# Kernel optimization log

Hardware: AMD Instinct MI355X
Metric: run time of the kernel (lower is better)

The kernel has to match this reference:

```python
import jax, jax.numpy as jnp
import numpy as np

B, S, D = 4, 2048, 1024  # batch, seq_len, isize; FFN hidden = isize, gate dim = 2*isize


def setup_inputs() -> dict:
    key = jax.random.key(0)
    ks = jax.random.split(key, 6)
    sc = lambda n: 1.0 / np.sqrt(n)
    return {
        "iQ": jax.random.normal(ks[0], (B, S, D), jnp.float32),
        "iV": jax.random.normal(ks[1], (B, S, D), jnp.float32),
        "W1": jax.random.normal(ks[2], (D, D), jnp.float32) * sc(D),
        "b1": jnp.zeros((D,), jnp.float32),
        "W2": jax.random.normal(ks[3], (D, D), jnp.float32) * sc(D),
        "b2": jnp.zeros((D,), jnp.float32),
        "Wg": jax.random.normal(ks[4], (2 * D, 2 * D), jnp.float32) * sc(2 * D),
        "bg": jnp.zeros((2 * D,), jnp.float32),
    }


def reference(iQ, iV, W1, b1, W2, b2, Wg, bg):
    seql = iV.shape[1]
    # AAN cumulative-average matrix: row i has 1/(i+1) in cols 0..i (lower triangular)
    inv = 1.0 / jnp.arange(1, seql + 1, dtype=iV.dtype)  # [S]
    attn = jnp.tril(jnp.broadcast_to(inv[:, None], (seql, seql)))  # [S, S]
    avg = jnp.einsum('st,btd->bsd', attn, iV)  # [B, S, D]
    # PositionwiseFF with norm_input=False, dropout=0: Linear -> ReLU -> Linear
    h = jax.nn.relu(avg @ W1 + b1)
    ffn = h @ W2 + b2  # [B, S, D]
    # sigmoid gate over concat(iQ, ffn)
    g = jax.nn.sigmoid(jnp.concatenate([iQ, ffn], axis=-1) @ Wg + bg)  # [B, S, 2D]
    d = ffn.shape[-1]
    igate = g[..., :d]
    fgate = g[..., d:]
    return igate * iQ + fgate * ffn
```

## Files before the change

kernel.cpp:

```cpp
#include <hip/hip_runtime.h>
#include <hip/hip_bf16.h>
#include <cstdint>

typedef unsigned short u16;
typedef unsigned int   u32;

typedef __attribute__((ext_vector_type(8))) short short8;
typedef __attribute__((ext_vector_type(4))) float f32x4;

__device__ __forceinline__ float b2f(u16 v) { return __uint_as_float(((u32)v) << 16); }
__device__ __forceinline__ u16 f2b(float f) {
    u32 u = __float_as_uint(f);
    u += 0x7FFFu + ((u >> 16) & 1u);
    return (u16)(u >> 16);
}

#define G2L16(gp, lp) __builtin_amdgcn_global_load_lds(                       \
    (const __attribute__((address_space(1))) void*)(gp),                      \
    (__attribute__((address_space(3))) void*)(lp), 16, 0, 0)

__device__ __forceinline__ void transpose_body(const float* __restrict__ in,
                                               u16* __restrict__ out,
                                               int R, int C, int lb, int tilesX,
                                               float (*tile)[33]) {
    const int bx = (lb % tilesX) * 32;
    const int by = (lb / tilesX) * 32;
    const int tx = threadIdx.x & 31, ty = threadIdx.x >> 5;
    #pragma unroll
    for (int i = 0; i < 32; i += 8)
        tile[ty + i][tx] = in[(size_t)(by + ty + i) * C + (bx + tx)];
    __syncthreads();
    #pragma unroll
    for (int i = 0; i < 32; i += 8)
        out[(size_t)(bx + ty + i) * R + (by + tx)] = f2b(tile[tx][ty + i]);
}

__global__ void prologue_kernel(const float* __restrict__ W1, u16* __restrict__ W1t,
                                const float* __restrict__ W2, u16* __restrict__ W2t,
                                const float* __restrict__ Wg, u16* __restrict__ Wgt,
                                const float* __restrict__ iQ, u16* __restrict__ iQb,
                                const float* __restrict__ iV, float* __restrict__ csum) {
    __shared__ float tile[32][33];
    const int bid = blockIdx.x;
    const int tid = threadIdx.x;
    if (bid < 1024) {
        transpose_body(W1, W1t, 1024, 1024, bid, 32, tile);
    } else if (bid < 2048) {
        transpose_body(W2, W2t, 1024, 1024, bid - 1024, 32, tile);
    } else if (bid < 6144) {
        transpose_body(Wg, Wgt, 2048, 2048, bid - 2048, 64, tile);
    } else if (bid < 14336) {
        const size_t i = ((size_t)(bid - 6144) * 256 + tid) * 4;
        const float4 v = *(const float4*)(iQ + i);
        ushort4 o;
        o.x = f2b(v.x); o.y = f2b(v.y); o.z = f2b(v.z); o.w = f2b(v.w);
        *(ushort4*)(iQb + i) = o;
    } else {
        const int idx = bid - 14336;
        const int b = idx >> 6, c = idx & 63;
        const int d = tid * 4;
        const float* src = iV + ((size_t)(b * 2048 + c * 32)) * 1024 + d;
        float4 s = {0.f, 0.f, 0.f, 0.f};
        #pragma unroll 8
        for (int i = 0; i < 32; ++i) {
            const float4 v = *(const float4*)(src + (size_t)i * 1024);
            s.x += v.x; s.y += v.y; s.z += v.z; s.w += v.w;
        }
        *(float4*)(csum + ((size_t)(b * 64 + c)) * 1024 + d) = s;
    }
}

__global__ void scan_kernel(const float* __restrict__ iV, const float* __restrict__ csum,
                            u16* __restrict__ avg) {
    const int c = blockIdx.x & 63, b = blockIdx.x >> 6;
    const int d = threadIdx.x * 4;
    float4 acc = {0.f, 0.f, 0.f, 0.f};
    const float* cs = csum + (size_t)b * 64 * 1024 + d;
    for (int cc = 0; cc < c; ++cc) {
        const float4 v = *(const float4*)(cs + (size_t)cc * 1024);
        acc.x += v.x; acc.y += v.y; acc.z += v.z; acc.w += v.w;
    }
    const size_t off = ((size_t)(b * 2048 + c * 32)) * 1024 + d;
    const float* src = iV + off;
    u16*         dst = avg + off;
    const int s0 = c * 32;
    #pragma unroll 4
    for (int i = 0; i < 32; ++i) {
        const float4 v = *(const float4*)(src + (size_t)i * 1024);
        acc.x += v.x; acc.y += v.y; acc.z += v.z; acc.w += v.w;
        const float inv = 1.0f / (float)(s0 + i + 1);
        ushort4 o;
        o.x = f2b(acc.x * inv); o.y = f2b(acc.y * inv);
        o.z = f2b(acc.z * inv); o.w = f2b(acc.w * inv);
        *(ushort4*)(dst + (size_t)i * 1024) = o;
    }
}

template <int EPI>
__global__ __launch_bounds__(256, 2)
void gemm_kernel(const u16* __restrict__ A, const u16* __restrict__ Bt,
                 const float* __restrict__ bias, u16* __restrict__ C,
                 int M, int N, int K) {
    __shared__ u16 As[128 * 32];
    __shared__ u16 Bs[128 * 32];

    const int tid  = threadIdx.x;
    const int m0   = blockIdx.x * 128;
    const int n0   = blockIdx.y * 128;
    const int wave = tid >> 6, lane = tid & 63;
    const int wm   = (wave & 1) << 6;
    const int wn   = (wave >> 1) << 6;
    const int quad = lane >> 4, l16 = lane & 15;

    f32x4 acc[4][4];
    #pragma unroll
    for (int i = 0; i < 4; ++i)
        #pragma unroll
        for (int j = 0; j < 4; ++j) acc[i][j] = (f32x4){0.f, 0.f, 0.f, 0.f};

    const int o1 = tid * 16, o2 = o1 + 4096;
    const int r1 = o1 >> 6, c1 = o1 & 63;
    const int r2 = o2 >> 6, c2 = o2 & 63;

    const int ktiles = K >> 5;
    for (int kt = 0; kt < ktiles; ++kt) {
        const int kb = kt << 5;
        const char* Ab = (const char*)(A + kb);
        const char* Bb = (const char*)(Bt + kb);
        G2L16(Ab + (size_t)(m0 + r1) * K * 2 + c1, (char*)As + o1);
        G2L16(Ab + (size_t)(m0 + r2) * K * 2 + c2, (char*)As + o2);
        G2L16(Bb + (size_t)(n0 + r1) * K * 2 + c1, (char*)Bs + o1);
        G2L16(Bb + (size_t)(n0 + r2) * K * 2 + c2, (char*)Bs + o2);
        __syncthreads();

        short8 af[4], bf[4];
        #pragma unroll
        for (int mi = 0; mi < 4; ++mi)
            af[mi] = *(const short8*)(As + (wm + mi * 16 + l16) * 32 + quad * 8);
        #pragma unroll
        for (int ni = 0; ni < 4; ++ni)
            bf[ni] = *(const short8*)(Bs + (wn + ni * 16 + l16) * 32 + quad * 8);
        #pragma unroll
        for (int mi = 0; mi < 4; ++mi)
            #pragma unroll
            for (int ni = 0; ni < 4; ++ni)
                acc[mi][ni] = __builtin_amdgcn_mfma_f32_16x16x32_bf16(
                    af[mi], bf[ni], acc[mi][ni], 0, 0, 0);
        __syncthreads();
    }

    #pragma unroll
    for (int ni = 0; ni < 4; ++ni) {
        const int col = n0 + wn + ni * 16 + l16;
        const float bv = bias[col];
        #pragma unroll
        for (int mi = 0; mi < 4; ++mi) {
            const int row0 = m0 + wm + mi * 16 + quad * 4;
            #pragma unroll
            for (int r = 0; r < 4; ++r) {
                float v = acc[mi][ni][r] + bv;
                if (EPI == 0) v = fmaxf(v, 0.f);
                C[(size_t)(row0 + r) * N + col] = f2b(v);
            }
        }
    }
}

__global__ __launch_bounds__(256, 2)
void gemm_gate_kernel(const u16* __restrict__ iQb, const u16* __restrict__ ffn,
                      const u16* __restrict__ Wgt, const float* __restrict__ bg,
                      const float* __restrict__ iQ, float* __restrict__ out,
                      int M, int D2 ) {
    __shared__ u16 As [128 * 32];
    __shared__ u16 Bs0[128 * 32];
    __shared__ u16 Bs1[128 * 32];

    const int tid  = threadIdx.x;
    const int m0   = blockIdx.x * 128;
    const int n0   = blockIdx.y * 128;
    const int wave = tid >> 6, lane = tid & 63;
    const int wm   = (wave & 1) << 6;
    const int wn   = (wave >> 1) << 6;
    const int quad = lane >> 4, l16 = lane & 15;
    const int D = D2 >> 1;

    f32x4 acc[2][4][4];
    #pragma unroll
    for (int p = 0; p < 2; ++p)
        #pragma unroll
        for (int i = 0; i < 4; ++i)
            #pragma unroll
            for (int j = 0; j < 4; ++j) acc[p][i][j] = (f32x4){0.f, 0.f, 0.f, 0.f};

    const int o1 = tid * 16, o2 = o1 + 4096;
    const int r1 = o1 >> 6, c1 = o1 & 63;
    const int r2 = o2 >> 6, c2 = o2 & 63;

    const int ktiles = D2 >> 5;
    for (int kt = 0; kt < ktiles; ++kt) {
        const int kb = kt << 5;
        const char* Ab = (const char*)((kb < D) ? (iQb + kb) : (ffn + (kb - D)));
        const char* B0 = (const char*)(Wgt + (size_t)n0 * D2 + kb);
        const char* B1 = (const char*)(Wgt + (size_t)(n0 + D) * D2 + kb);
        G2L16(Ab + (size_t)(m0 + r1) * D * 2 + c1, (char*)As + o1);
        G2L16(Ab + (size_t)(m0 + r2) * D * 2 + c2, (char*)As + o2);
        G2L16(B0 + (size_t)r1 * D2 * 2 + c1, (char*)Bs0 + o1);
        G2L16(B0 + (size_t)r2 * D2 * 2 + c2, (char*)Bs0 + o2);
        G2L16(B1 + (size_t)r1 * D2 * 2 + c1, (char*)Bs1 + o1);
        G2L16(B1 + (size_t)r2 * D2 * 2 + c2, (char*)Bs1 + o2);
        __syncthreads();

        short8 af[4], bf0[4], bf1[4];
        #pragma unroll
        for (int mi = 0; mi < 4; ++mi)
            af[mi] = *(const short8*)(As + (wm + mi * 16 + l16) * 32 + quad * 8);
        #pragma unroll
        for (int ni = 0; ni < 4; ++ni) {
            bf0[ni] = *(const short8*)(Bs0 + (wn + ni * 16 + l16) * 32 + quad * 8);
            bf1[ni] = *(const short8*)(Bs1 + (wn + ni * 16 + l16) * 32 + quad * 8);
        }
        #pragma unroll
        for (int mi = 0; mi < 4; ++mi)
            #pragma unroll
            for (int ni = 0; ni < 4; ++ni) {
                acc[0][mi][ni] = __builtin_amdgcn_mfma_f32_16x16x32_bf16(
                    af[mi], bf0[ni], acc[0][mi][ni], 0, 0, 0);
                acc[1][mi][ni] = __builtin_amdgcn_mfma_f32_16x16x32_bf16(
                    af[mi], bf1[ni], acc[1][mi][ni], 0, 0, 0);
            }
        __syncthreads();
    }

    #pragma unroll
    for (int ni = 0; ni < 4; ++ni) {
        const int col = n0 + wn + ni * 16 + l16;
        const float bgi = bg[col];
        const float bgf = bg[col + D];
        #pragma unroll
        for (int mi = 0; mi < 4; ++mi) {
            const int row0 = m0 + wm + mi * 16 + quad * 4;
            #pragma unroll
            for (int r = 0; r < 4; ++r) {
                const size_t idx = (size_t)(row0 + r) * D + col;
                const float gi = 1.0f / (1.0f + __expf(-(acc[0][mi][ni][r] + bgi)));
                const float gf = 1.0f / (1.0f + __expf(-(acc[1][mi][ni][r] + bgf)));
                out[idx] = gi * iQ[idx] + gf * b2f(ffn[idx]);
            }
        }
    }
}

extern "C" void kernel_launch(void* const* d_in, const int* in_sizes, int n_in,
                              void* d_out, int out_size, void* d_ws, size_t ws_size,
                              hipStream_t stream) {
    const int B = 4, S = 2048, D = 1024, D2 = 2048;
    const int M = B * S;

    const float* iQ = (const float*)d_in[0];
    const float* iV = (const float*)d_in[1];
    const float* W1 = (const float*)d_in[2];
    const float* b1 = (const float*)d_in[3];
    const float* W2 = (const float*)d_in[4];
    const float* b2 = (const float*)d_in[5];
    const float* Wg = (const float*)d_in[6];
    const float* bg = (const float*)d_in[7];
    float* out = (float*)d_out;

    u16*   regA = (u16*)d_ws;
    u16*   regB = regA + (size_t)M * D;
    u16*   iQb  = regB + (size_t)M * D;
    u16*   W1t  = iQb  + (size_t)M * D;
    u16*   W2t  = W1t  + (size_t)D * D;
    u16*   Wgt  = W2t  + (size_t)D * D;
    float* csum = (float*)(Wgt + (size_t)D2 * D2);

    u16* avg = regA;
    u16* ffn = regA;
    u16* h   = regB;

    prologue_kernel<<<14592, 256, 0, stream>>>(W1, W1t, W2, W2t, Wg, Wgt,
                                               iQ, iQb, iV, csum);
    scan_kernel<<<B * 64, 256, 0, stream>>>(iV, csum, avg);
    gemm_kernel<0><<<dim3(M / 128, D / 128), 256, 0, stream>>>(avg, W1t, b1, h, M, D, D);
    gemm_kernel<1><<<dim3(M / 128, D / 128), 256, 0, stream>>>(h, W2t, b2, ffn, M, D, D);
    gemm_gate_kernel<<<dim3(M / 128, D / 128), 256, 0, stream>>>(
        iQb, ffn, Wgt, bg, iQ, out, M, D2);
}
```

Before: 304.3 us.

## Double GEMM K-tile to 64 with XOR-swizzled LDS layout; unroll scan prefix

Both GEMM kernels now stage 64-wide K tiles instead of 32, which halves the number of barrier pairs per K loop. The shared-memory layout uses an XOR swizzle on 16-byte chunks so that MFMA fragment reads avoid bank conflicts. The scan kernel's chunk-prefix loop gets four independent accumulators to expose more memory-level parallelism. In exchange, LDS use doubles, reaching 48KB for the gate kernel, which may limit the two-blocks-per-CU occupancy.

```diff
diff --git a/kernel.cpp b/kernel.cpp
--- a/kernel.cpp
+++ b/kernel.cpp
@@ -74,12 +74,29 @@
                             u16* __restrict__ avg) {
     const int c = blockIdx.x & 63, b = blockIdx.x >> 6;
     const int d = threadIdx.x * 4;
-    float4 acc = {0.f, 0.f, 0.f, 0.f};
     const float* cs = csum + (size_t)b * 64 * 1024 + d;
-    for (int cc = 0; cc < c; ++cc) {
+    float4 a0 = {0,0,0,0}, a1 = {0,0,0,0}, a2 = {0,0,0,0}, a3 = {0,0,0,0};
+    int cc = 0;
+    for (; cc + 4 <= c; cc += 4) {
+        const float4 v0 = *(const float4*)(cs + (size_t)(cc + 0) * 1024);
+        const float4 v1 = *(const float4*)(cs + (size_t)(cc + 1) * 1024);
+        const float4 v2 = *(const float4*)(cs + (size_t)(cc + 2) * 1024);
+        const float4 v3 = *(const float4*)(cs + (size_t)(cc + 3) * 1024);
+        a0.x += v0.x; a0.y += v0.y; a0.z += v0.z; a0.w += v0.w;
+        a1.x += v1.x; a1.y += v1.y; a1.z += v1.z; a1.w += v1.w;
+        a2.x += v2.x; a2.y += v2.y; a2.z += v2.z; a2.w += v2.w;
+        a3.x += v3.x; a3.y += v3.y; a3.z += v3.z; a3.w += v3.w;
+    }
+    for (; cc < c; ++cc) {
         const float4 v = *(const float4*)(cs + (size_t)cc * 1024);
-        acc.x += v.x; acc.y += v.y; acc.z += v.z; acc.w += v.w;
-    }
+        a0.x += v.x; a0.y += v.y; a0.z += v.z; a0.w += v.w;
+    }
+    float4 acc;
+    acc.x = (a0.x + a1.x) + (a2.x + a3.x);
+    acc.y = (a0.y + a1.y) + (a2.y + a3.y);
+    acc.z = (a0.z + a1.z) + (a2.z + a3.z);
+    acc.w = (a0.w + a1.w) + (a2.w + a3.w);
+
     const size_t off = ((size_t)(b * 2048 + c * 32)) * 1024 + d;
     const float* src = iV + off;
     u16*         dst = avg + off;
@@ -101,8 +118,8 @@
 void gemm_kernel(const u16* __restrict__ A, const u16* __restrict__ Bt,
                  const float* __restrict__ bias, u16* __restrict__ C,
                  int M, int N, int K) {
-    __shared__ u16 As[128 * 32];
-    __shared__ u16 Bs[128 * 32];
+    __shared__ u16 As[128 * 64];
+    __shared__ u16 Bs[128 * 64];
 
     const int tid  = threadIdx.x;
     const int m0   = blockIdx.x * 128;
@@ -118,34 +135,46 @@
         #pragma unroll
         for (int j = 0; j < 4; ++j) acc[i][j] = (f32x4){0.f, 0.f, 0.f, 0.f};
 
-    const int o1 = tid * 16, o2 = o1 + 4096;
-    const int r1 = o1 >> 6, c1 = o1 & 63;
-    const int r2 = o2 >> 6, c2 = o2 & 63;
-
-    const int ktiles = K >> 5;
+    int oo[4], rr[4], qq[4];
+    #pragma unroll
+    for (int j = 0; j < 4; ++j) {
+        oo[j] = tid * 16 + j * 4096;
+        rr[j] = oo[j] >> 7;
+        qq[j] = ((oo[j] >> 4) & 7) ^ (rr[j] & 7);
+    }
+
+    const int ktiles = K >> 6;
     for (int kt = 0; kt < ktiles; ++kt) {
-        const int kb = kt << 5;
-        const char* Ab = (const char*)(A + kb);
-        const char* Bb = (const char*)(Bt + kb);
-        G2L16(Ab + (size_t)(m0 + r1) * K * 2 + c1, (char*)As + o1);
-        G2L16(Ab + (size_t)(m0 + r2) * K * 2 + c2, (char*)As + o2);
-        G2L16(Bb + (size_t)(n0 + r1) * K * 2 + c1, (char*)Bs + o1);
-        G2L16(Bb + (size_t)(n0 + r2) * K * 2 + c2, (char*)Bs + o2);
+        const int kb = kt << 6;
+        #pragma unroll
+        for (int j = 0; j < 4; ++j) {
+            G2L16((const char*)A  + ((size_t)(m0 + rr[j]) * K + kb) * 2 + qq[j] * 16,
+                  (char*)As + oo[j]);
+            G2L16((const char*)Bt + ((size_t)(n0 + rr[j]) * K + kb) * 2 + qq[j] * 16,
+                  (char*)Bs + oo[j]);
+        }
         __syncthreads();
 
-        short8 af[4], bf[4];
-        #pragma unroll
-        for (int mi = 0; mi < 4; ++mi)
-            af[mi] = *(const short8*)(As + (wm + mi * 16 + l16) * 32 + quad * 8);
-        #pragma unroll
-        for (int ni = 0; ni < 4; ++ni)
-            bf[ni] = *(const short8*)(Bs + (wn + ni * 16 + l16) * 32 + quad * 8);
-        #pragma unroll
-        for (int mi = 0; mi < 4; ++mi)
-            #pragma unroll
-            for (int ni = 0; ni < 4; ++ni)
-                acc[mi][ni] = __builtin_amdgcn_mfma_f32_16x16x32_bf16(
-                    af[mi], bf[ni], acc[mi][ni], 0, 0, 0);
+        #pragma unroll
+        for (int h = 0; h < 2; ++h) {
+            short8 af[4], bf[4];
+            #pragma unroll
+            for (int mi = 0; mi < 4; ++mi) {
+                const int R = wm + mi * 16 + l16;
+                af[mi] = *(const short8*)(As + R * 64 + ((((h << 2) | quad) ^ (R & 7)) << 3));
+            }
+            #pragma unroll
+            for (int ni = 0; ni < 4; ++ni) {
+                const int R = wn + ni * 16 + l16;
+                bf[ni] = *(const short8*)(Bs + R * 64 + ((((h << 2) | quad) ^ (R & 7)) << 3));
+            }
+            #pragma unroll
+            for (int mi = 0; mi < 4; ++mi)
+                #pragma unroll
+                for (int ni = 0; ni < 4; ++ni)
+                    acc[mi][ni] = __builtin_amdgcn_mfma_f32_16x16x32_bf16(
+                        af[mi], bf[ni], acc[mi][ni], 0, 0, 0);
+        }
         __syncthreads();
     }
 
@@ -171,9 +200,9 @@
                       const u16* __restrict__ Wgt, const float* __restrict__ bg,
                       const float* __restrict__ iQ, float* __restrict__ out,
                       int M, int D2 ) {
-    __shared__ u16 As [128 * 32];
-    __shared__ u16 Bs0[128 * 32];
-    __shared__ u16 Bs1[128 * 32];
+    __shared__ u16 As [128 * 64];
+    __shared__ u16 Bs0[128 * 64];
+    __shared__ u16 Bs1[128 * 64];
 
     const int tid  = threadIdx.x;
     const int m0   = blockIdx.x * 128;
@@ -192,42 +221,53 @@
             #pragma unroll
             for (int j = 0; j < 4; ++j) acc[p][i][j] = (f32x4){0.f, 0.f, 0.f, 0.f};
 
-    const int o1 = tid * 16, o2 = o1 + 4096;
-    const int r1 = o1 >> 6, c1 = o1 & 63;
-    const int r2 = o2 >> 6, c2 = o2 & 63;
-
-    const int ktiles = D2 >> 5;
+    int oo[4], rr[4], qq[4];
+    #pragma unroll
+    for (int j = 0; j < 4; ++j) {
+        oo[j] = tid * 16 + j * 4096;
+        rr[j] = oo[j] >> 7;
+        qq[j] = ((oo[j] >> 4) & 7) ^ (rr[j] & 7);
+    }
+
+    const int ktiles = D2 >> 6;
     for (int kt = 0; kt < ktiles; ++kt) {
-        const int kb = kt << 5;
+        const int kb = kt << 6;
         const char* Ab = (const char*)((kb < D) ? (iQb + kb) : (ffn + (kb - D)));
         const char* B0 = (const char*)(Wgt + (size_t)n0 * D2 + kb);
         const char* B1 = (const char*)(Wgt + (size_t)(n0 + D) * D2 + kb);
-        G2L16(Ab + (size_t)(m0 + r1) * D * 2 + c1, (char*)As + o1);
-        G2L16(Ab + (size_t)(m0 + r2) * D * 2 + c2, (char*)As + o2);
-        G2L16(B0 + (size_t)r1 * D2 * 2 + c1, (char*)Bs0 + o1);
-        G2L16(B0 + (size_t)r2 * D2 * 2 + c2, (char*)Bs0 + o2);
-        G2L16(B1 + (size_t)r1 * D2 * 2 + c1, (char*)Bs1 + o1);
-        G2L16(B1 + (size_t)r2 * D2 * 2 + c2, (char*)Bs1 + o2);
+        #pragma unroll
+        for (int j = 0; j < 4; ++j) {
+            G2L16(Ab + (size_t)(m0 + rr[j]) * D * 2 + qq[j] * 16, (char*)As  + oo[j]);
+            G2L16(B0 + (size_t)rr[j] * D2 * 2 + qq[j] * 16,       (char*)Bs0 + oo[j]);
+            G2L16(B1 + (size_t)rr[j] * D2 * 2 + qq[j] * 16,       (char*)Bs1 + oo[j]);
+        }
         __syncthreads();
 
-        short8 af[4], bf0[4], bf1[4];
-        #pragma unroll
-        for (int mi = 0; mi < 4; ++mi)
-            af[mi] = *(const short8*)(As + (wm + mi * 16 + l16) * 32 + quad * 8);
-        #pragma unroll
-        for (int ni = 0; ni < 4; ++ni) {
-            bf0[ni] = *(const short8*)(Bs0 + (wn + ni * 16 + l16) * 32 + quad * 8);
-            bf1[ni] = *(const short8*)(Bs1 + (wn + ni * 16 + l16) * 32 + quad * 8);
-        }
-        #pragma unroll
-        for (int mi = 0; mi < 4; ++mi)
+        #pragma unroll
+        for (int h = 0; h < 2; ++h) {
+            short8 af[4], bf0[4], bf1[4];
+            #pragma unroll
+            for (int mi = 0; mi < 4; ++mi) {
+                const int R = wm + mi * 16 + l16;
+                af[mi] = *(const short8*)(As + R * 64 + ((((h << 2) | quad) ^ (R & 7)) << 3));
+            }
             #pragma unroll
             for (int ni = 0; ni < 4; ++ni) {
-                acc[0][mi][ni] = __builtin_amdgcn_mfma_f32_16x16x32_bf16(
-                    af[mi], bf0[ni], acc[0][mi][ni], 0, 0, 0);
-                acc[1][mi][ni] = __builtin_amdgcn_mfma_f32_16x16x32_bf16(
-                    af[mi], bf1[ni], acc[1][mi][ni], 0, 0, 0);
-            }
+                const int R = wn + ni * 16 + l16;
+                const int so = R * 64 + ((((h << 2) | quad) ^ (R & 7)) << 3);
+                bf0[ni] = *(const short8*)(Bs0 + so);
+                bf1[ni] = *(const short8*)(Bs1 + so);
+            }
+            #pragma unroll
+            for (int mi = 0; mi < 4; ++mi)
+                #pragma unroll
+                for (int ni = 0; ni < 4; ++ni) {
+                    acc[0][mi][ni] = __builtin_amdgcn_mfma_f32_16x16x32_bf16(
+                        af[mi], bf0[ni], acc[0][mi][ni], 0, 0, 0);
+                    acc[1][mi][ni] = __builtin_amdgcn_mfma_f32_16x16x32_bf16(
+                        af[mi], bf1[ni], acc[1][mi][ni], 0, 0, 0);
+                }
+        }
         __syncthreads();
     }
 
```

Result: faster. 267.8 us (-12.0%).
